# Kernel tuning notes

Hardware: AMD Instinct MI355X
Metric: run time of the kernel (lower is better)

Reference implementation:

```python
import jax, jax.numpy as jnp
import numpy as np
import math

RANKS = [16, 8, 4, 2, 1]          # generate_mrlora_ranks(32 // 2)
LORA_ALPHA = 16.0
SCALES = [LORA_ALPHA / math.sqrt(r) for r in RANKS]  # use_rslora=True
D_IN = 4096
D_OUT = 4096


def setup_inputs() -> dict:
    key = jax.random.key(0)
    ks = jax.random.split(key, 3 + 2 * len(RANKS))
    x = jax.random.normal(ks[0], (4, 2048, D_IN), dtype=jnp.float32)
    W = jax.random.normal(ks[1], (D_OUT, D_IN), dtype=jnp.float32) * (1.0 / math.sqrt(D_IN))
    b = jax.random.normal(ks[2], (D_OUT,), dtype=jnp.float32) * 0.01
    inp = {"x": x, "W": W, "b": b}
    for i, r in enumerate(RANKS):
        # A: [r, D_IN], B: [D_OUT, r] (torch nn.Linear weight layout)
        inp[f"A{r}"] = jax.random.normal(ks[3 + 2 * i], (r, D_IN), dtype=jnp.float32) * (1.0 / math.sqrt(D_IN))
        inp[f"B{r}"] = jax.random.normal(ks[4 + 2 * i], (D_OUT, r), dtype=jnp.float32) * 0.02
    inp["alphas"] = jnp.ones((len(RANKS),), dtype=jnp.float32)
    return inp


def reference(x, W, b, A16, B16, A8, B8, A4, B4, A2, B2, A1, B1, alphas):
    # base linear: x @ W.T + b
    out = jnp.einsum('bsd,od->bso', x, W) + b
    As = [A16, A8, A4, A2, A1]
    Bs = [B16, B8, B4, B2, B1]
    # dropout p=0 -> identity; per-rank low-rank update with learned + rslora scale
    for i, (A, B) in enumerate(zip(As, Bs)):
        coef = alphas[i] * SCALES[i]
        out = out + coef * jnp.einsum('bsr,or->bso', jnp.einsum('bsd,rd->bsr', x, A), B)
    return out
```

## Files before the change

kernel.cpp:

```cpp
#include <hip/hip_runtime.h>
#include <hip/hip_bf16.h>
#include <stdint.h>

#define DK 4096
#define MROWS 8192
#define NOUT 4096
#define KP 4160
#define KP_B (KP*2)
#define NT 65

typedef __attribute__((ext_vector_type(8))) __bf16 bf16x8;
typedef __attribute__((ext_vector_type(4))) float f32x4;
typedef unsigned short u16;

struct __align__(8) us4 { u16 x, y, z, w; };

__device__ __forceinline__ u16 f2bf(float f) {
  union { float f; uint32_t u; } v; v.f = f;
  uint32_t r = v.u + 0x7fffu + ((v.u >> 16) & 1u);
  return (u16)(r >> 16);
}

__device__ __forceinline__ void gload16(const void* g, void* l) {
  __builtin_amdgcn_global_load_lds(
      (const __attribute__((address_space(1))) unsigned int*)g,
      (__attribute__((address_space(3))) unsigned int*)l, 16, 0, 0);
}

__global__ void build_W(const float* __restrict__ W,
                        const float* __restrict__ B16, const float* __restrict__ B8,
                        const float* __restrict__ B4,  const float* __restrict__ B2,
                        const float* __restrict__ B1,  const float* __restrict__ alphas,
                        u16* __restrict__ wb) {
  int n = blockIdx.x, t = threadIdx.x;
  const float* src = W + (size_t)n * DK;
  u16* dst = wb + (size_t)n * KP;
#pragma unroll
  for (int j = 0; j < 4; ++j) {
    int col = (t + j * 256) * 4;
    float4 v = *reinterpret_cast<const float4*>(src + col);
    us4 o = { f2bf(v.x), f2bf(v.y), f2bf(v.z), f2bf(v.w) };
    *reinterpret_cast<us4*>(dst + col) = o;
  }
  if (t < 64) {
    u16 val = 0;
    if (t < 31) {
      float coef; const float* Bp; int r, rl;
      if (t < 16)      { coef = alphas[0] * 4.0f;                Bp = B16; r = 16; rl = t; }
      else if (t < 24) { coef = alphas[1] * 5.656854249492381f;  Bp = B8;  r = 8;  rl = t - 16; }
      else if (t < 28) { coef = alphas[2] * 8.0f;                Bp = B4;  r = 4;  rl = t - 24; }
      else if (t < 30) { coef = alphas[3] * 11.313708498984761f; Bp = B2;  r = 2;  rl = t - 28; }
      else             { coef = alphas[4] * 16.0f;               Bp = B1;  r = 1;  rl = 0; }
      val = f2bf(coef * Bp[(size_t)n * r + rl]);
    }
    dst[4096 + t] = val;
  }
}

__global__ void build_A(const float* __restrict__ A16, const float* __restrict__ A8,
                        const float* __restrict__ A4,  const float* __restrict__ A2,
                        const float* __restrict__ A1,  u16* __restrict__ ab) {
  int rr = blockIdx.x, t = threadIdx.x;
  const float* src = nullptr;
  if (rr < 16)      src = A16 + (size_t)rr * DK;
  else if (rr < 24) src = A8 + (size_t)(rr - 16) * DK;
  else if (rr < 28) src = A4 + (size_t)(rr - 24) * DK;
  else if (rr < 30) src = A2 + (size_t)(rr - 28) * DK;
  else if (rr < 31) src = A1;
  u16* dst = ab + (size_t)rr * DK;
#pragma unroll
  for (int j = 0; j < 4; ++j) {
    int col = (t + j * 256) * 4;
    us4 o = { 0, 0, 0, 0 };
    if (src) {
      float4 v = *reinterpret_cast<const float4*>(src + col);
      o = { f2bf(v.x), f2bf(v.y), f2bf(v.z), f2bf(v.w) };
    }
    *reinterpret_cast<us4*>(dst + col) = o;
  }
}

__global__ __launch_bounds__(256, 2) void conv_xa(const float* __restrict__ x, u16* __restrict__ xb,
                                                  const u16* __restrict__ ab) {
  __shared__ float part[4][2][64][4];
  int m0 = blockIdx.x * 16;
  int t = threadIdx.x, lane = t & 63, w = t >> 6;
  int l15 = lane & 15, lg = lane >> 4;
  int row = m0 + l15;
  const float* xp = x + (size_t)row * DK + w * 1024 + lg * 8;
  u16* xbp = xb + (size_t)row * KP + w * 1024 + lg * 8;
  const u16* a0 = ab + (size_t)l15 * DK + w * 1024 + lg * 8;
  const u16* a1 = ab + (size_t)(16 + l15) * DK + w * 1024 + lg * 8;
  f32x4 acc0 = {}, acc1 = {};
  union { bf16x8 v; us4 h[2]; } xf;
#pragma unroll 4
  for (int kk = 0; kk < 32; ++kk) {
    float4 v0 = *reinterpret_cast<const float4*>(xp + kk * 32);
    float4 v1 = *reinterpret_cast<const float4*>(xp + kk * 32 + 4);
    xf.h[0] = us4{ f2bf(v0.x), f2bf(v0.y), f2bf(v0.z), f2bf(v0.w) };
    xf.h[1] = us4{ f2bf(v1.x), f2bf(v1.y), f2bf(v1.z), f2bf(v1.w) };
    *reinterpret_cast<us4*>(xbp + kk * 32) = xf.h[0];
    *reinterpret_cast<us4*>(xbp + kk * 32 + 4) = xf.h[1];
    bf16x8 af0 = *reinterpret_cast<const bf16x8*>(a0 + kk * 32);
    bf16x8 af1 = *reinterpret_cast<const bf16x8*>(a1 + kk * 32);
    acc0 = __builtin_amdgcn_mfma_f32_16x16x32_bf16(xf.v, af0, acc0, 0, 0, 0);
    acc1 = __builtin_amdgcn_mfma_f32_16x16x32_bf16(xf.v, af1, acc1, 0, 0, 0);
  }
  *reinterpret_cast<f32x4*>(&part[w][0][lane][0]) = acc0;
  *reinterpret_cast<f32x4*>(&part[w][1][lane][0]) = acc1;
  __syncthreads();
  if (w == 0) {
#pragma unroll
    for (int ni = 0; ni < 2; ++ni) {
      f32x4 s = *reinterpret_cast<const f32x4*>(&part[0][ni][lane][0]);
#pragma unroll
      for (int ww = 1; ww < 4; ++ww)
        s += *reinterpret_cast<const f32x4*>(&part[ww][ni][lane][0]);
#pragma unroll
      for (int r = 0; r < 4; ++r)
        xb[(size_t)(m0 + lg * 4 + r) * KP + 4096 + ni * 16 + l15] = f2bf(s[r]);
    }
  }
  if (t < 128) {
    us4 z = { 0, 0, 0, 0 };
    *reinterpret_cast<us4*>(xb + (size_t)(m0 + (t >> 3)) * KP + 4128 + (t & 7) * 4) = z;
  }
}

__device__ __forceinline__ void stage_tile(const char* gbase, char* lbase, int w, int lane, int i) {
  int chunk = (w << 2) + i;
  int row = (chunk << 3) + (lane >> 3);
  int src_c = ((lane & 7) ^ (lane >> 3)) << 4;
  gload16(gbase + (size_t)row * KP_B + src_c, lbase + chunk * 1024);
}

__device__ __forceinline__ bf16x8 rdfrag(const char* base, int row, int cb) {
  return *reinterpret_cast<const bf16x8*>(base + row * 128 + (cb ^ ((row & 7) << 4)));
}

__global__ __launch_bounds__(512, 2) void gemm_main(const u16* __restrict__ xb, const u16* __restrict__ wb,
                                                    const float* __restrict__ bias, float* __restrict__ out) {
  __shared__ u16 As0[256 * 64], As1[256 * 64];
  __shared__ u16 Bs0[256 * 64], Bs1[256 * 64];
  int bid = blockIdx.x;
  int swz = (bid & 7) * 64 + (bid >> 3);
  int mt = swz >> 4, nt = swz & 15;
  int m0 = mt * 256, n0 = nt * 256;
  int t = threadIdx.x, lane = t & 63, w = t >> 6;
  int wr = w >> 2, wc = w & 3;
  int l15 = lane & 15, lg = lane >> 4;

  f32x4 acc[8][4] = {};
  bf16x8 af[4][2], af2[4][2], bl[2][2], bh[2][2];

  const char* Ag = (const char*)xb + (size_t)m0 * KP_B;
  const char* Bg = (const char*)wb + (size_t)n0 * KP_B;
  char *AcA = (char*)As0, *AnA = (char*)As1, *AcB = (char*)Bs0, *AnB = (char*)Bs1;

#pragma unroll
  for (int i = 0; i < 4; ++i) stage_tile(Ag, AcA, w, lane, i);
#pragma unroll
  for (int i = 0; i < 4; ++i) stage_tile(Bg, AcB, w, lane, i);
  asm volatile("s_waitcnt vmcnt(0)" ::: "memory");
  __builtin_amdgcn_s_barrier();

  const int Arow = wr * 128 + l15;
  const int Brow = wc * 64 + l15;
  const int cb0 = lg * 16;

  for (int kt = 0; kt < NT; ++kt) {
    const char* Agk1 = Ag + (size_t)(kt + 1) * 128;
    const char* Bgk1 = Bg + (size_t)(kt + 1) * 128;
    const bool doS = (kt + 1 < NT);

#pragma unroll
    for (int mi = 0; mi < 4; ++mi)
#pragma unroll
      for (int ks = 0; ks < 2; ++ks)
        af[mi][ks] = rdfrag(AcA, Arow + mi * 16, cb0 + ks * 64);
#pragma unroll
    for (int ni = 0; ni < 2; ++ni)
#pragma unroll
      for (int ks = 0; ks < 2; ++ks)
        bl[ni][ks] = rdfrag(AcB, Brow + ni * 16, cb0 + ks * 64);
    if (doS) {
      stage_tile(Agk1, AnA, w, lane, 0); stage_tile(Agk1, AnA, w, lane, 1);
      stage_tile(Agk1, AnA, w, lane, 2); stage_tile(Agk1, AnA, w, lane, 3);
    }

#pragma unroll
    for (int ni = 0; ni < 2; ++ni)
#pragma unroll
      for (int ks = 0; ks < 2; ++ks)
        bh[ni][ks] = rdfrag(AcB, Brow + 32 + ni * 16, cb0 + ks * 64);
    if (doS) {
      stage_tile(Bgk1, AnB, w, lane, 0); stage_tile(Bgk1, AnB, w, lane, 1);
      stage_tile(Bgk1, AnB, w, lane, 2); stage_tile(Bgk1, AnB, w, lane, 3);
    }
    asm volatile("s_waitcnt lgkmcnt(4)" ::: "memory");
    __builtin_amdgcn_sched_barrier(0);
    __builtin_amdgcn_s_setprio(1);
#pragma unroll
    for (int mi = 0; mi < 4; ++mi)
#pragma unroll
      for (int ni = 0; ni < 2; ++ni)
#pragma unroll
        for (int ks = 0; ks < 2; ++ks)
          acc[mi][ni] = __builtin_amdgcn_mfma_f32_16x16x32_bf16(af[mi][ks], bl[ni][ks], acc[mi][ni], 0, 0, 0);
    __builtin_amdgcn_s_setprio(0);

#pragma unroll
    for (int mi = 0; mi < 4; ++mi)
#pragma unroll
      for (int ks = 0; ks < 2; ++ks)
        af2[mi][ks] = rdfrag(AcA, Arow + 64 + mi * 16, cb0 + ks * 64);
    asm volatile("s_waitcnt lgkmcnt(8)" ::: "memory");
    __builtin_amdgcn_sched_barrier(0);
    __builtin_amdgcn_s_setprio(1);
#pragma unroll
    for (int mi = 0; mi < 4; ++mi)
#pragma unroll
      for (int ni = 0; ni < 2; ++ni)
#pragma unroll
        for (int ks = 0; ks < 2; ++ks)
          acc[mi][ni + 2] = __builtin_amdgcn_mfma_f32_16x16x32_bf16(af[mi][ks], bh[ni][ks], acc[mi][ni + 2], 0, 0, 0);
    __builtin_amdgcn_s_setprio(0);

    asm volatile("s_waitcnt lgkmcnt(0)" ::: "memory");
    __builtin_amdgcn_sched_barrier(0);
    __builtin_amdgcn_s_setprio(1);
#pragma unroll
    for (int mi = 0; mi < 4; ++mi)
#pragma unroll
      for (int ni = 0; ni < 2; ++ni)
#pragma unroll
        for (int ks = 0; ks < 2; ++ks)
          acc[mi + 4][ni + 2] = __builtin_amdgcn_mfma_f32_16x16x32_bf16(af2[mi][ks], bh[ni][ks], acc[mi + 4][ni + 2], 0, 0, 0);
    __builtin_amdgcn_s_setprio(0);

    __builtin_amdgcn_s_setprio(1);
#pragma unroll
    for (int mi = 0; mi < 4; ++mi)
#pragma unroll
      for (int ni = 0; ni < 2; ++ni)
#pragma unroll
        for (int ks = 0; ks < 2; ++ks)
          acc[mi + 4][ni] = __builtin_amdgcn_mfma_f32_16x16x32_bf16(af2[mi][ks], bl[ni][ks], acc[mi + 4][ni], 0, 0, 0);
    __builtin_amdgcn_s_setprio(0);
    asm volatile("s_waitcnt vmcnt(0)" ::: "memory");
    __builtin_amdgcn_s_barrier();

    { char* tp = AcA; AcA = AnA; AnA = tp; }
    { char* tp = AcB; AcB = AnB; AnB = tp; }
  }

  float bn[4];
#pragma unroll
  for (int ni = 0; ni < 4; ++ni) bn[ni] = bias[n0 + wc * 64 + ni * 16 + l15];
#pragma unroll
  for (int mi = 0; mi < 8; ++mi) {
    int mbase = m0 + wr * 128 + mi * 16 + lg * 4;
#pragma unroll
    for (int ni = 0; ni < 4; ++ni) {
      int n = n0 + wc * 64 + ni * 16 + l15;
#pragma unroll
      for (int r = 0; r < 4; ++r)
        out[(size_t)(mbase + r) * NOUT + n] = acc[mi][ni][r] + bn[ni];
    }
  }
}

extern "C" void kernel_launch(void* const* d_in, const int* in_sizes, int n_in,
                              void* d_out, int out_size, void* d_ws, size_t ws_size,
                              hipStream_t stream) {
  const float* x   = (const float*)d_in[0];
  const float* W   = (const float*)d_in[1];
  const float* b   = (const float*)d_in[2];
  const float* A16 = (const float*)d_in[3];
  const float* B16 = (const float*)d_in[4];
  const float* A8  = (const float*)d_in[5];
  const float* B8  = (const float*)d_in[6];
  const float* A4  = (const float*)d_in[7];
  const float* B4  = (const float*)d_in[8];
  const float* A2  = (const float*)d_in[9];
  const float* B2  = (const float*)d_in[10];
  const float* A1  = (const float*)d_in[11];
  const float* B1  = (const float*)d_in[12];
  const float* alphas = (const float*)d_in[13];

  char* ws = (char*)d_ws;
  u16* xb = (u16*)ws;
  u16* wb = (u16*)(ws + 68157440);
  u16* ab = (u16*)(ws + 68157440 + 34078720);
  float* out = (float*)d_out;

  build_A<<<32, 256, 0, stream>>>(A16, A8, A4, A2, A1, ab);
  conv_xa<<<MROWS / 16, 256, 0, stream>>>(x, xb, ab);
  build_W<<<NOUT, 256, 0, stream>>>(W, B16, B8, B4, B2, B1, alphas, wb);
  gemm_main<<<(MROWS / 256) * (NOUT / 256), 512, 0, stream>>>(xb, wb, b, out);
}
```

Before: 293.7 us.

## Load A fragments directly from global into registers, bypassing LDS

Removes the shared-memory staging of the x (A) tile and instead has each wave load its MFMA A-fragments straight from global memory into registers, prefetching the next k-step's low half during compute. The MFMA phases are reordered and the vmcnt wait is relaxed to overlap these direct loads with the B-tile LDS staging. This halves LDS usage and removes the A ds_read traffic. In exchange, each wave issues its own uncoalesced 16-byte global loads and the A data is no longer shared across the four column waves, which raises global/L2 traffic and can expose load latency.

```diff
diff --git a/kernel.cpp b/kernel.cpp
--- a/kernel.cpp
+++ b/kernel.cpp
@@ -140,7 +140,6 @@
 
 __global__ __launch_bounds__(512, 2) void gemm_main(const u16* __restrict__ xb, const u16* __restrict__ wb,
                                                     const float* __restrict__ bias, float* __restrict__ out) {
-  __shared__ u16 As0[256 * 64], As1[256 * 64];
   __shared__ u16 Bs0[256 * 64], Bs1[256 * 64];
   int bid = blockIdx.x;
   int swz = (bid & 7) * 64 + (bid >> 3);
@@ -153,46 +152,50 @@
   f32x4 acc[8][4] = {};
   bf16x8 af[4][2], af2[4][2], bl[2][2], bh[2][2];
 
-  const char* Ag = (const char*)xb + (size_t)m0 * KP_B;
   const char* Bg = (const char*)wb + (size_t)n0 * KP_B;
-  char *AcA = (char*)As0, *AnA = (char*)As1, *AcB = (char*)Bs0, *AnB = (char*)Bs1;
-
-#pragma unroll
-  for (int i = 0; i < 4; ++i) stage_tile(Ag, AcA, w, lane, i);
+  char *AcB = (char*)Bs0, *AnB = (char*)Bs1;
+
+  const u16 *pAlo[4], *pAhi[4];
+#pragma unroll
+  for (int mi = 0; mi < 4; ++mi) {
+    size_t r = (size_t)(m0 + wr * 128 + mi * 16 + l15) * KP + lg * 8;
+    pAlo[mi] = xb + r;
+    pAhi[mi] = xb + r + (size_t)64 * KP;
+  }
+
+#pragma unroll
+  for (int mi = 0; mi < 4; ++mi)
+#pragma unroll
+    for (int ks = 0; ks < 2; ++ks)
+      af[mi][ks] = *reinterpret_cast<const bf16x8*>(pAlo[mi] + ks * 32);
 #pragma unroll
   for (int i = 0; i < 4; ++i) stage_tile(Bg, AcB, w, lane, i);
   asm volatile("s_waitcnt vmcnt(0)" ::: "memory");
   __builtin_amdgcn_s_barrier();
 
-  const int Arow = wr * 128 + l15;
   const int Brow = wc * 64 + l15;
   const int cb0 = lg * 16;
 
   for (int kt = 0; kt < NT; ++kt) {
-    const char* Agk1 = Ag + (size_t)(kt + 1) * 128;
     const char* Bgk1 = Bg + (size_t)(kt + 1) * 128;
     const bool doS = (kt + 1 < NT);
 
 #pragma unroll
-    for (int mi = 0; mi < 4; ++mi)
-#pragma unroll
-      for (int ks = 0; ks < 2; ++ks)
-        af[mi][ks] = rdfrag(AcA, Arow + mi * 16, cb0 + ks * 64);
-#pragma unroll
     for (int ni = 0; ni < 2; ++ni)
 #pragma unroll
       for (int ks = 0; ks < 2; ++ks)
         bl[ni][ks] = rdfrag(AcB, Brow + ni * 16, cb0 + ks * 64);
-    if (doS) {
-      stage_tile(Agk1, AnA, w, lane, 0); stage_tile(Agk1, AnA, w, lane, 1);
-      stage_tile(Agk1, AnA, w, lane, 2); stage_tile(Agk1, AnA, w, lane, 3);
-    }
-
 #pragma unroll
     for (int ni = 0; ni < 2; ++ni)
 #pragma unroll
       for (int ks = 0; ks < 2; ++ks)
         bh[ni][ks] = rdfrag(AcB, Brow + 32 + ni * 16, cb0 + ks * 64);
+
+#pragma unroll
+    for (int mi = 0; mi < 4; ++mi)
+#pragma unroll
+      for (int ks = 0; ks < 2; ++ks)
+        af2[mi][ks] = *reinterpret_cast<const bf16x8*>(pAhi[mi] + ks * 32);
     if (doS) {
       stage_tile(Bgk1, AnB, w, lane, 0); stage_tile(Bgk1, AnB, w, lane, 1);
       stage_tile(Bgk1, AnB, w, lane, 2); stage_tile(Bgk1, AnB, w, lane, 3);
@@ -209,23 +212,6 @@
           acc[mi][ni] = __builtin_amdgcn_mfma_f32_16x16x32_bf16(af[mi][ks], bl[ni][ks], acc[mi][ni], 0, 0, 0);
     __builtin_amdgcn_s_setprio(0);
 
-#pragma unroll
-    for (int mi = 0; mi < 4; ++mi)
-#pragma unroll
-      for (int ks = 0; ks < 2; ++ks)
-        af2[mi][ks] = rdfrag(AcA, Arow + 64 + mi * 16, cb0 + ks * 64);
-    asm volatile("s_waitcnt lgkmcnt(8)" ::: "memory");
-    __builtin_amdgcn_sched_barrier(0);
-    __builtin_amdgcn_s_setprio(1);
-#pragma unroll
-    for (int mi = 0; mi < 4; ++mi)
-#pragma unroll
-      for (int ni = 0; ni < 2; ++ni)
-#pragma unroll
-        for (int ks = 0; ks < 2; ++ks)
-          acc[mi][ni + 2] = __builtin_amdgcn_mfma_f32_16x16x32_bf16(af[mi][ks], bh[ni][ks], acc[mi][ni + 2], 0, 0, 0);
-    __builtin_amdgcn_s_setprio(0);
-
     asm volatile("s_waitcnt lgkmcnt(0)" ::: "memory");
     __builtin_amdgcn_sched_barrier(0);
     __builtin_amdgcn_s_setprio(1);
@@ -235,6 +221,23 @@
       for (int ni = 0; ni < 2; ++ni)
 #pragma unroll
         for (int ks = 0; ks < 2; ++ks)
+          acc[mi][ni + 2] = __builtin_amdgcn_mfma_f32_16x16x32_bf16(af[mi][ks], bh[ni][ks], acc[mi][ni + 2], 0, 0, 0);
+    __builtin_amdgcn_s_setprio(0);
+
+    if (doS) {
+#pragma unroll
+      for (int mi = 0; mi < 4; ++mi)
+#pragma unroll
+        for (int ks = 0; ks < 2; ++ks)
+          af[mi][ks] = *reinterpret_cast<const bf16x8*>(pAlo[mi] + 64 + ks * 32);
+    }
+    __builtin_amdgcn_s_setprio(1);
+#pragma unroll
+    for (int mi = 0; mi < 4; ++mi)
+#pragma unroll
+      for (int ni = 0; ni < 2; ++ni)
+#pragma unroll
+        for (int ks = 0; ks < 2; ++ks)
           acc[mi + 4][ni + 2] = __builtin_amdgcn_mfma_f32_16x16x32_bf16(af2[mi][ks], bh[ni][ks], acc[mi + 4][ni + 2], 0, 0, 0);
     __builtin_amdgcn_s_setprio(0);
 
@@ -247,10 +250,12 @@
         for (int ks = 0; ks < 2; ++ks)
           acc[mi + 4][ni] = __builtin_amdgcn_mfma_f32_16x16x32_bf16(af2[mi][ks], bl[ni][ks], acc[mi + 4][ni], 0, 0, 0);
     __builtin_amdgcn_s_setprio(0);
-    asm volatile("s_waitcnt vmcnt(0)" ::: "memory");
+#pragma unroll
+    for (int mi = 0; mi < 4; ++mi) { pAlo[mi] += 64; pAhi[mi] += 64; }
+    if (kt < NT - 1) asm volatile("s_waitcnt vmcnt(8)" ::: "memory");
+    else             asm volatile("s_waitcnt vmcnt(0)" ::: "memory");
     __builtin_amdgcn_s_barrier();
 
-    { char* tp = AcA; AcA = AnA; AnA = tp; }
     { char* tp = AcB; AcB = AnB; AnB = tp; }
   }
 
```

Measured after the change: 675.4 us. 130% more time.

## Shrink GEMM block tile to 128x256 with BK=32 and four waves

Applied to the files above, without the earlier changes.

Reworks the main GEMM from 256x256 tiles with 8 waves and a K-step of 64 to 128x256 tiles with 4 waves and a K-step of 32. The LDS staging layout and swizzle change to match 64-byte rows, and the grid doubles to 1024 blocks. The aim is a smaller LDS footprint and more blocks per CU for better occupancy and wave balance. In exchange, arithmetic intensity per block drops, the K loop runs twice as many iterations, and each iteration pays its own barrier.

```diff
diff --git a/kernel.cpp b/kernel.cpp
--- a/kernel.cpp
+++ b/kernel.cpp
@@ -7,7 +7,7 @@
 #define NOUT 4096
 #define KP 4160
 #define KP_B (KP*2)
-#define NT 65
+#define NT2 130
 
 typedef __attribute__((ext_vector_type(8))) __bf16 bf16x8;
 typedef __attribute__((ext_vector_type(4))) float f32x4;
@@ -127,125 +127,80 @@
   }
 }
 
-__device__ __forceinline__ void stage_tile(const char* gbase, char* lbase, int w, int lane, int i) {
-  int chunk = (w << 2) + i;
-  int row = (chunk << 3) + (lane >> 3);
-  int src_c = ((lane & 7) ^ (lane >> 3)) << 4;
-  gload16(gbase + (size_t)row * KP_B + src_c, lbase + chunk * 1024);
-}
-
-__device__ __forceinline__ bf16x8 rdfrag(const char* base, int row, int cb) {
-  return *reinterpret_cast<const bf16x8*>(base + row * 128 + (cb ^ ((row & 7) << 4)));
-}
-
-__global__ __launch_bounds__(512, 2) void gemm_main(const u16* __restrict__ xb, const u16* __restrict__ wb,
+__device__ __forceinline__ void stage_rc(const char* gbase, char* lbase, int t, int i) {
+  int row = i * 64 + (t >> 2);
+  int src_c = ((t & 3) ^ ((row >> 1) & 3)) << 4;
+  gload16(gbase + (size_t)row * KP_B + src_c, lbase + i * 4096 + t * 16);
+}
+
+__device__ __forceinline__ bf16x8 rdfrag(const char* base, int row, int lg) {
+  return *reinterpret_cast<const bf16x8*>(base + row * 64 + ((lg ^ ((row >> 1) & 3)) << 4));
+}
+
+__global__ __launch_bounds__(256, 2) void gemm_main(const u16* __restrict__ xb, const u16* __restrict__ wb,
                                                     const float* __restrict__ bias, float* __restrict__ out) {
-  __shared__ u16 As0[256 * 64], As1[256 * 64];
-  __shared__ u16 Bs0[256 * 64], Bs1[256 * 64];
+  __shared__ u16 As0[128 * 32], As1[128 * 32];
+  __shared__ u16 Bs0[256 * 32], Bs1[256 * 32];
   int bid = blockIdx.x;
-  int swz = (bid & 7) * 64 + (bid >> 3);
+  int swz = (bid & 7) * 128 + (bid >> 3);
   int mt = swz >> 4, nt = swz & 15;
-  int m0 = mt * 256, n0 = nt * 256;
+  int m0 = mt * 128, n0 = nt * 256;
   int t = threadIdx.x, lane = t & 63, w = t >> 6;
-  int wr = w >> 2, wc = w & 3;
   int l15 = lane & 15, lg = lane >> 4;
 
   f32x4 acc[8][4] = {};
-  bf16x8 af[4][2], af2[4][2], bl[2][2], bh[2][2];
+  bf16x8 af[8], b[4];
 
   const char* Ag = (const char*)xb + (size_t)m0 * KP_B;
   const char* Bg = (const char*)wb + (size_t)n0 * KP_B;
   char *AcA = (char*)As0, *AnA = (char*)As1, *AcB = (char*)Bs0, *AnB = (char*)Bs1;
 
-#pragma unroll
-  for (int i = 0; i < 4; ++i) stage_tile(Ag, AcA, w, lane, i);
-#pragma unroll
-  for (int i = 0; i < 4; ++i) stage_tile(Bg, AcB, w, lane, i);
+  stage_rc(Ag, AcA, t, 0); stage_rc(Ag, AcA, t, 1);
+#pragma unroll
+  for (int i = 0; i < 4; ++i) stage_rc(Bg, AcB, t, i);
   asm volatile("s_waitcnt vmcnt(0)" ::: "memory");
   __builtin_amdgcn_s_barrier();
 
-  const int Arow = wr * 128 + l15;
-  const int Brow = wc * 64 + l15;
-  const int cb0 = lg * 16;
-
-  for (int kt = 0; kt < NT; ++kt) {
-    const char* Agk1 = Ag + (size_t)(kt + 1) * 128;
-    const char* Bgk1 = Bg + (size_t)(kt + 1) * 128;
-    const bool doS = (kt + 1 < NT);
-
-#pragma unroll
-    for (int mi = 0; mi < 4; ++mi)
-#pragma unroll
-      for (int ks = 0; ks < 2; ++ks)
-        af[mi][ks] = rdfrag(AcA, Arow + mi * 16, cb0 + ks * 64);
+  const int Brow0 = w * 64 + l15;
+
+  for (int kt = 0; kt < NT2; ++kt) {
+    const char* Agk1 = Ag + (size_t)(kt + 1) * 64;
+    const char* Bgk1 = Bg + (size_t)(kt + 1) * 64;
+    const bool doS = (kt + 1 < NT2);
+
+#pragma unroll
+    for (int mi = 0; mi < 8; ++mi)
+      af[mi] = rdfrag(AcA, mi * 16 + l15, lg);
 #pragma unroll
     for (int ni = 0; ni < 2; ++ni)
-#pragma unroll
-      for (int ks = 0; ks < 2; ++ks)
-        bl[ni][ks] = rdfrag(AcB, Brow + ni * 16, cb0 + ks * 64);
+      b[ni] = rdfrag(AcB, Brow0 + ni * 16, lg);
+    if (doS) { stage_rc(Agk1, AnA, t, 0); stage_rc(Agk1, AnA, t, 1); }
+
+#pragma unroll
+    for (int ni = 2; ni < 4; ++ni)
+      b[ni] = rdfrag(AcB, Brow0 + ni * 16, lg);
     if (doS) {
-      stage_tile(Agk1, AnA, w, lane, 0); stage_tile(Agk1, AnA, w, lane, 1);
-      stage_tile(Agk1, AnA, w, lane, 2); stage_tile(Agk1, AnA, w, lane, 3);
-    }
-
-#pragma unroll
-    for (int ni = 0; ni < 2; ++ni)
-#pragma unroll
-      for (int ks = 0; ks < 2; ++ks)
-        bh[ni][ks] = rdfrag(AcB, Brow + 32 + ni * 16, cb0 + ks * 64);
-    if (doS) {
-      stage_tile(Bgk1, AnB, w, lane, 0); stage_tile(Bgk1, AnB, w, lane, 1);
-      stage_tile(Bgk1, AnB, w, lane, 2); stage_tile(Bgk1, AnB, w, lane, 3);
-    }
-    asm volatile("s_waitcnt lgkmcnt(4)" ::: "memory");
+      stage_rc(Bgk1, AnB, t, 0); stage_rc(Bgk1, AnB, t, 1);
+      stage_rc(Bgk1, AnB, t, 2); stage_rc(Bgk1, AnB, t, 3);
+    }
+    asm volatile("s_waitcnt lgkmcnt(2)" ::: "memory");
     __builtin_amdgcn_sched_barrier(0);
     __builtin_amdgcn_s_setprio(1);
 #pragma unroll
-    for (int mi = 0; mi < 4; ++mi)
+    for (int mi = 0; mi < 8; ++mi)
 #pragma unroll
       for (int ni = 0; ni < 2; ++ni)
-#pragma unroll
-        for (int ks = 0; ks < 2; ++ks)
-          acc[mi][ni] = __builtin_amdgcn_mfma_f32_16x16x32_bf16(af[mi][ks], bl[ni][ks], acc[mi][ni], 0, 0, 0);
-    __builtin_amdgcn_s_setprio(0);
-
-#pragma unroll
-    for (int mi = 0; mi < 4; ++mi)
-#pragma unroll
-      for (int ks = 0; ks < 2; ++ks)
-        af2[mi][ks] = rdfrag(AcA, Arow + 64 + mi * 16, cb0 + ks * 64);
-    asm volatile("s_waitcnt lgkmcnt(8)" ::: "memory");
-    __builtin_amdgcn_sched_barrier(0);
-    __builtin_amdgcn_s_setprio(1);
-#pragma unroll
-    for (int mi = 0; mi < 4; ++mi)
-#pragma unroll
-      for (int ni = 0; ni < 2; ++ni)
-#pragma unroll
-        for (int ks = 0; ks < 2; ++ks)
-          acc[mi][ni + 2] = __builtin_amdgcn_mfma_f32_16x16x32_bf16(af[mi][ks], bh[ni][ks], acc[mi][ni + 2], 0, 0, 0);
+        acc[mi][ni] = __builtin_amdgcn_mfma_f32_16x16x32_bf16(af[mi], b[ni], acc[mi][ni], 0, 0, 0);
     __builtin_amdgcn_s_setprio(0);
 
     asm volatile("s_waitcnt lgkmcnt(0)" ::: "memory");
     __builtin_amdgcn_sched_barrier(0);
     __builtin_amdgcn_s_setprio(1);
 #pragma unroll
-    for (int mi = 0; mi < 4; ++mi)
-#pragma unroll
-      for (int ni = 0; ni < 2; ++ni)
-#pragma unroll
-        for (int ks = 0; ks < 2; ++ks)
-          acc[mi + 4][ni + 2] = __builtin_amdgcn_mfma_f32_16x16x32_bf16(af2[mi][ks], bh[ni][ks], acc[mi + 4][ni + 2], 0, 0, 0);
-    __builtin_amdgcn_s_setprio(0);
-
-    __builtin_amdgcn_s_setprio(1);
-#pragma unroll
-    for (int mi = 0; mi < 4; ++mi)
-#pragma unroll
-      for (int ni = 0; ni < 2; ++ni)
-#pragma unroll
-        for (int ks = 0; ks < 2; ++ks)
-          acc[mi + 4][ni] = __builtin_amdgcn_mfma_f32_16x16x32_bf16(af2[mi][ks], bl[ni][ks], acc[mi + 4][ni], 0, 0, 0);
+    for (int mi = 0; mi < 8; ++mi)
+#pragma unroll
+      for (int ni = 2; ni < 4; ++ni)
+        acc[mi][ni] = __builtin_amdgcn_mfma_f32_16x16x32_bf16(af[mi], b[ni], acc[mi][ni], 0, 0, 0);
     __builtin_amdgcn_s_setprio(0);
     asm volatile("s_waitcnt vmcnt(0)" ::: "memory");
     __builtin_amdgcn_s_barrier();
@@ -256,13 +211,13 @@
 
   float bn[4];
 #pragma unroll
-  for (int ni = 0; ni < 4; ++ni) bn[ni] = bias[n0 + wc * 64 + ni * 16 + l15];
+  for (int ni = 0; ni < 4; ++ni) bn[ni] = bias[n0 + w * 64 + ni * 16 + l15];
 #pragma unroll
   for (int mi = 0; mi < 8; ++mi) {
-    int mbase = m0 + wr * 128 + mi * 16 + lg * 4;
+    int mbase = m0 + mi * 16 + lg * 4;
 #pragma unroll
     for (int ni = 0; ni < 4; ++ni) {
-      int n = n0 + wc * 64 + ni * 16 + l15;
+      int n = n0 + w * 64 + ni * 16 + l15;
 #pragma unroll
       for (int r = 0; r < 4; ++r)
         out[(size_t)(mbase + r) * NOUT + n] = acc[mi][ni][r] + bn[ni];
@@ -297,5 +252,5 @@
   build_A<<<32, 256, 0, stream>>>(A16, A8, A4, A2, A1, ab);
   conv_xa<<<MROWS / 16, 256, 0, stream>>>(x, xb, ab);
   build_W<<<NOUT, 256, 0, stream>>>(W, B16, B8, B4, B2, B1, alphas, wb);
-  gemm_main<<<(MROWS / 256) * (NOUT / 256), 512, 0, stream>>>(xb, wb, b, out);
-}
+  gemm_main<<<(MROWS / 128) * (NOUT / 256), 256, 0, stream>>>(xb, wb, b, out);
+}
```

Result: slower. 328.8 us (+11.9%).

## Triple-buffer B tiles to prefetch two K-steps ahead

Applied to the files above, without the earlier changes.

Adds a third LDS buffer for the weight tile and issues B loads two iterations ahead, waiting only on the older loads (vmcnt(4)) so one B tile stays in flight across the barrier. This hides more global-load latency for B. The extra 32KB of LDS forces launch bounds down to one block per CU, which lowers occupancy and cross-block latency hiding.

```diff
diff --git a/kernel.cpp b/kernel.cpp
--- a/kernel.cpp
+++ b/kernel.cpp
@@ -138,10 +138,10 @@
   return *reinterpret_cast<const bf16x8*>(base + row * 128 + (cb ^ ((row & 7) << 4)));
 }
 
-__global__ __launch_bounds__(512, 2) void gemm_main(const u16* __restrict__ xb, const u16* __restrict__ wb,
+__global__ __launch_bounds__(512, 1) void gemm_main(const u16* __restrict__ xb, const u16* __restrict__ wb,
                                                     const float* __restrict__ bias, float* __restrict__ out) {
   __shared__ u16 As0[256 * 64], As1[256 * 64];
-  __shared__ u16 Bs0[256 * 64], Bs1[256 * 64];
+  __shared__ u16 Bs0[256 * 64], Bs1[256 * 64], Bs2[256 * 64];
   int bid = blockIdx.x;
   int swz = (bid & 7) * 64 + (bid >> 3);
   int mt = swz >> 4, nt = swz & 15;
@@ -155,13 +155,16 @@
 
   const char* Ag = (const char*)xb + (size_t)m0 * KP_B;
   const char* Bg = (const char*)wb + (size_t)n0 * KP_B;
-  char *AcA = (char*)As0, *AnA = (char*)As1, *AcB = (char*)Bs0, *AnB = (char*)Bs1;
+  char *AcA = (char*)As0, *AnA = (char*)As1;
+  char *Br0 = (char*)Bs0, *Br1 = (char*)Bs1, *Br2 = (char*)Bs2;
 
 #pragma unroll
   for (int i = 0; i < 4; ++i) stage_tile(Ag, AcA, w, lane, i);
 #pragma unroll
-  for (int i = 0; i < 4; ++i) stage_tile(Bg, AcB, w, lane, i);
-  asm volatile("s_waitcnt vmcnt(0)" ::: "memory");
+  for (int i = 0; i < 4; ++i) stage_tile(Bg, Br0, w, lane, i);
+#pragma unroll
+  for (int i = 0; i < 4; ++i) stage_tile(Bg + 128, Br1, w, lane, i);
+  asm volatile("s_waitcnt vmcnt(4)" ::: "memory");
   __builtin_amdgcn_s_barrier();
 
   const int Arow = wr * 128 + l15;
@@ -170,8 +173,8 @@
 
   for (int kt = 0; kt < NT; ++kt) {
     const char* Agk1 = Ag + (size_t)(kt + 1) * 128;
-    const char* Bgk1 = Bg + (size_t)(kt + 1) * 128;
-    const bool doS = (kt + 1 < NT);
+    const char* Bgk2 = Bg + (size_t)(kt + 2) * 128;
+    const bool doA = (kt + 1 < NT), doB = (kt + 2 < NT);
 
 #pragma unroll
     for (int mi = 0; mi < 4; ++mi)
@@ -182,8 +185,8 @@
     for (int ni = 0; ni < 2; ++ni)
 #pragma unroll
       for (int ks = 0; ks < 2; ++ks)
-        bl[ni][ks] = rdfrag(AcB, Brow + ni * 16, cb0 + ks * 64);
-    if (doS) {
+        bl[ni][ks] = rdfrag(Br0, Brow + ni * 16, cb0 + ks * 64);
+    if (doA) {
       stage_tile(Agk1, AnA, w, lane, 0); stage_tile(Agk1, AnA, w, lane, 1);
       stage_tile(Agk1, AnA, w, lane, 2); stage_tile(Agk1, AnA, w, lane, 3);
     }
@@ -192,10 +195,10 @@
     for (int ni = 0; ni < 2; ++ni)
 #pragma unroll
       for (int ks = 0; ks < 2; ++ks)
-        bh[ni][ks] = rdfrag(AcB, Brow + 32 + ni * 16, cb0 + ks * 64);
-    if (doS) {
-      stage_tile(Bgk1, AnB, w, lane, 0); stage_tile(Bgk1, AnB, w, lane, 1);
-      stage_tile(Bgk1, AnB, w, lane, 2); stage_tile(Bgk1, AnB, w, lane, 3);
+        bh[ni][ks] = rdfrag(Br0, Brow + 32 + ni * 16, cb0 + ks * 64);
+    if (doB) {
+      stage_tile(Bgk2, Br2, w, lane, 0); stage_tile(Bgk2, Br2, w, lane, 1);
+      stage_tile(Bgk2, Br2, w, lane, 2); stage_tile(Bgk2, Br2, w, lane, 3);
     }
     asm volatile("s_waitcnt lgkmcnt(4)" ::: "memory");
     __builtin_amdgcn_sched_barrier(0);
@@ -247,11 +250,12 @@
         for (int ks = 0; ks < 2; ++ks)
           acc[mi + 4][ni] = __builtin_amdgcn_mfma_f32_16x16x32_bf16(af2[mi][ks], bl[ni][ks], acc[mi + 4][ni], 0, 0, 0);
     __builtin_amdgcn_s_setprio(0);
-    asm volatile("s_waitcnt vmcnt(0)" ::: "memory");
+    if (kt < NT - 2) asm volatile("s_waitcnt vmcnt(4)" ::: "memory");
+    else             asm volatile("s_waitcnt vmcnt(0)" ::: "memory");
     __builtin_amdgcn_s_barrier();
 
     { char* tp = AcA; AcA = AnA; AnA = tp; }
-    { char* tp = AcB; AcB = AnB; AnB = tp; }
+    { char* tp = Br0; Br0 = Br1; Br1 = Br2; Br2 = tp; }
   }
 
   float bn[4];
```

New measurement: 297.1 us. No clear change (+1.2%).
